# Performance work log

Hardware: AMD Instinct MI355X
Metric: run time of the kernel (lower is better)

## Reference

```python
import jax, jax.numpy as jnp
import numpy as np

N = 200000
E = 400000
H = 256
L = 4
FEAT = 10
NUM_BOND_TYPES = 4
VOCAB = 100


def _layernorm(x, g, b, eps=1e-5):
    mu = jnp.mean(x, axis=-1, keepdims=True)
    var = jnp.var(x, axis=-1, keepdims=True)
    return (x - mu) * jax.lax.rsqrt(var + eps) * g + b


def setup_inputs() -> dict:
    key = jax.random.key(0)
    ks = jax.random.split(key, 20)
    s = 0.05
    return {
        "z": jax.random.randint(ks[0], (N,), 0, VOCAB),
        "feat": jax.random.normal(ks[1], (N, FEAT), jnp.float32),
        "edge_index": jax.random.randint(ks[2], (2, E), 0, N),
        "edge_attr": jax.random.uniform(ks[3], (E, NUM_BOND_TYPES), jnp.float32),
        "batch": jnp.sort(jax.random.randint(ks[4], (N,), 0, 512)),
        "emb": jax.random.normal(ks[5], (VOCAB, H), jnp.float32) * s,
        "Wf": jax.random.normal(ks[6], (FEAT, H), jnp.float32) * s,
        "bf": jnp.zeros((H,), jnp.float32),
        "g0": jnp.ones((H,), jnp.float32),
        "b0": jnp.zeros((H,), jnp.float32),
        "We": jax.random.normal(ks[7], (NUM_BOND_TYPES, H), jnp.float32) * s,
        "be": jnp.zeros((H,), jnp.float32),
        "W1": jax.random.normal(ks[8], (L, H, H), jnp.float32) * s,
        "b1": jnp.zeros((L, H), jnp.float32),
        "W2": jax.random.normal(ks[9], (L, H, H), jnp.float32) * s,
        "b2": jnp.zeros((L, H), jnp.float32),
        "ln_g": jnp.ones((L, H), jnp.float32),
        "ln_b": jnp.zeros((L, H), jnp.float32),
    }


def reference(z, feat, edge_index, edge_attr, batch, emb, Wf, bf, g0, b0,
              We, be, W1, b1, W2, b2, ln_g, ln_b):
    act = jax.nn.silu
    # node embedding: silu(Emb[z] + feat @ Wf + bf) -> LayerNorm
    x = _layernorm(act(emb[z] + feat @ Wf + bf), g0, b0)  # [N, H]
    # edge feature projection: silu(edge_attr @ We + be)
    e = act(edge_attr @ We + be)  # [E, H]
    src, dst = edge_index[0], edge_index[1]
    for l in range(L):
        # GINEConv message: relu(x_j + e_ij), sum-aggregated at destination
        m = jax.nn.relu(x[src] + e)  # [E, H]
        agg = jax.ops.segment_sum(m, dst, num_segments=N)  # [N, H]
        h = agg + x  # eps = 0
        h = act(h @ W1[l] + b1[l]) @ W2[l] + b2[l]
        x = _layernorm(x + h, ln_g[l], ln_b[l])
    return x, batch
```

## Files before the change

kernel.cpp:

```cpp
#include <hip/hip_runtime.h>
#include <hip/hip_bf16.h>

#define NN 200000
#define EE 400000
#define HDIM 256
#define LL 4
#define FEAT 10

typedef unsigned short ushort_t;
typedef unsigned char uchar_t;
typedef __attribute__((ext_vector_type(8))) short bf16x8;
typedef __attribute__((ext_vector_type(8))) unsigned short u16x8;
typedef __attribute__((ext_vector_type(2))) float f32x2;
typedef __attribute__((ext_vector_type(4))) float f32x4;
typedef __attribute__((ext_vector_type(4))) unsigned int u32x4;

__device__ inline ushort_t f2bf(float f) {
    unsigned int u = __builtin_bit_cast(unsigned int, f);
    return (ushort_t)((u + 0x7fffu + ((u >> 16) & 1u)) >> 16);
}
__device__ inline float bf2f(ushort_t s) {
    unsigned int u = ((unsigned int)s) << 16;
    return __builtin_bit_cast(float, u);
}
__device__ inline float silu_f(float v) { return v / (1.0f + __expf(-v)); }

__device__ inline void x8_load(const void* base, size_t idx, float* f) {
    uint2 v = ((const uint2*)base)[idx];
    f32x2 a0 = __builtin_amdgcn_cvt_pk_f32_fp8((int)v.x, false);
    f32x2 a1 = __builtin_amdgcn_cvt_pk_f32_fp8((int)v.x, true);
    f32x2 a2 = __builtin_amdgcn_cvt_pk_f32_fp8((int)v.y, false);
    f32x2 a3 = __builtin_amdgcn_cvt_pk_f32_fp8((int)v.y, true);
    f[0]=a0[0]; f[1]=a0[1]; f[2]=a1[0]; f[3]=a1[1];
    f[4]=a2[0]; f[5]=a2[1]; f[6]=a3[0]; f[7]=a3[1];
}
__device__ inline void x8_store(void* base, size_t idx, const float* f) {
    int t0 = __builtin_amdgcn_cvt_pk_fp8_f32(f[0], f[1], 0, false);
    t0 = __builtin_amdgcn_cvt_pk_fp8_f32(f[2], f[3], t0, true);
    int t1 = __builtin_amdgcn_cvt_pk_fp8_f32(f[4], f[5], 0, false);
    t1 = __builtin_amdgcn_cvt_pk_fp8_f32(f[6], f[7], t1, true);
    uint2 o; o.x = (unsigned int)t0; o.y = (unsigned int)t1;
    ((uint2*)base)[idx] = o;
}

__global__ __launch_bounds__(256) void prep_wf_kernel(
    const float* __restrict__ Wf, ushort_t* __restrict__ Wfc)
{
    int idx = blockIdx.x * 256 + threadIdx.x;
    if (idx >= 8192) return;
    int e = idx & 7;
    int lane = (idx >> 3) & 63;
    int nf = (idx >> 9) & 1;
    int w8 = idx >> 10;
    int n = w8 * 32 + nf * 16 + (lane & 15);
    int k = (lane >> 4) * 8 + e;
    Wfc[idx] = (k < FEAT) ? f2bf(Wf[k * HDIM + n]) : (ushort_t)0;
}

__global__ __launch_bounds__(512, 4) void node_init_kernel(
    const int* __restrict__ z, const float* __restrict__ feat,
    const float* __restrict__ emb, const ushort_t* __restrict__ Wfc,
    const float* __restrict__ bfv, const float* __restrict__ g0,
    const float* __restrict__ b0, void* __restrict__ xb)
{
    __shared__ ushort_t sA[64][256];
    __shared__ float sGB[2][HDIM];
    const int tid = threadIdx.x;
    const int m0 = blockIdx.x * 64;
    const int lane = tid & 63;
    const int w = tid >> 6;
    const int lg = lane >> 4, ll = lane & 15;
    const int cb = w * 32;

    if (tid < HDIM) sGB[0][tid] = g0[tid];
    else sGB[1][tid - HDIM] = b0[tid - HDIM];

    f32x4 bvv[2];
    #pragma unroll
    for (int nf = 0; nf < 2; ++nf)
        bvv[nf] = *(const f32x4*)&bfv[cb + nf * 16 + lg * 4];

    bf16x8 wf[2];
    wf[0] = *(const bf16x8*)(Wfc + w * 1024 + lane * 8);
    wf[1] = *(const bf16x8*)(Wfc + w * 1024 + 512 + lane * 8);

    bf16x8 af[4];
    #pragma unroll
    for (int m = 0; m < 4; ++m) {
        int gr = m0 + m * 16 + ll;
        bf16x8 t = {};
        if (lg == 0) {
            #pragma unroll
            for (int j = 0; j < 8; ++j) t[j] = (short)f2bf(feat[gr * FEAT + j]);
        } else if (lg == 1) {
            t[0] = (short)f2bf(feat[gr * FEAT + 8]);
            t[1] = (short)f2bf(feat[gr * FEAT + 9]);
        }
        af[m] = t;
    }

    f32x4 acc[4][2] = {};
    #pragma unroll
    for (int m = 0; m < 4; ++m)
        #pragma unroll
        for (int nf = 0; nf < 2; ++nf)
            acc[m][nf] = __builtin_amdgcn_mfma_f32_16x16x32_bf16(
                wf[nf], af[m], acc[m][nf], 0, 0, 0);

    #pragma unroll
    for (int m = 0; m < 4; ++m) {
        int r = m * 16 + ll, rx = r & 7;
        int zi = z[m0 + r];
        #pragma unroll
        for (int nf = 0; nf < 2; ++nf) {
            int n0 = cb + nf * 16 + lg * 4;
            f32x4 ev = *(const f32x4*)&emb[(size_t)zi * HDIM + n0];
            int chunk = ((cb + nf * 16) >> 3) + (lg >> 1);
            int celloff = ((chunk ^ rx) << 3) + (lg & 1) * 4;
            ushort4 o;
            o.x = f2bf(silu_f(acc[m][nf][0] + ev[0] + bvv[nf][0]));
            o.y = f2bf(silu_f(acc[m][nf][1] + ev[1] + bvv[nf][1]));
            o.z = f2bf(silu_f(acc[m][nf][2] + ev[2] + bvv[nf][2]));
            o.w = f2bf(silu_f(acc[m][nf][3] + ev[3] + bvv[nf][3]));
            *(ushort4*)&sA[r][celloff] = o;
        }
    }
    __syncthreads();

    {
        int rr = tid >> 3, kk = tid & 7;
        int rot = (kk + rr) & 7;
        u16x8 v8[4];
        float s = 0.f, q = 0.f;
        #pragma unroll
        for (int i = 0; i < 4; ++i) {
            int slot = rot + 8 * i;
            v8[i] = *(const u16x8*)&sA[rr][slot << 3];
            #pragma unroll
            for (int j = 0; j < 8; ++j) {
                float v = bf2f(v8[i][j]);
                s += v; q += v * v;
            }
        }
        #pragma unroll
        for (int o = 1; o < 8; o <<= 1) {
            s += __shfl_xor(s, o, 64);
            q += __shfl_xor(q, o, 64);
        }
        float mu = s * (1.0f / HDIM);
        float var = q * (1.0f / HDIM) - mu * mu;
        float rs = rsqrtf(var + 1e-5f);
        size_t rows = ((size_t)(m0 + rr)) << 5;
        #pragma unroll
        for (int i = 0; i < 4; ++i) {
            int slot = rot + 8 * i;
            int chunk = slot ^ (rr & 7);
            float ov[8];
            #pragma unroll
            for (int j = 0; j < 8; ++j)
                ov[j] = (bf2f(v8[i][j]) - mu) * rs * sGB[0][chunk * 8 + j]
                        + sGB[1][chunk * 8 + j];
            x8_store(xb, rows + slot, ov);
        }
    }
}

__global__ __launch_bounds__(256) void batch_out_kernel(
    const int* __restrict__ batch, float* __restrict__ out)
{
    int i = blockIdx.x * 256 + threadIdx.x;
    if (i < NN) out[i] = (float)batch[i];
}

__global__ __launch_bounds__(256) void hist_kernel(const int* __restrict__ ei, int* __restrict__ deg)
{
    int i = blockIdx.x * 256 + threadIdx.x;
    if (i < EE) atomicAdd(&deg[ei[EE + i]], 1);
}

__global__ __launch_bounds__(256) void scan_blocks_kernel(
    const int* __restrict__ deg, int* __restrict__ off, int* __restrict__ psum)
{
    int blk = blockIdx.x, t = threadIdx.x;
    int base = blk * 1024 + t * 4;
    int v[4];
    #pragma unroll
    for (int i = 0; i < 4; ++i) v[i] = (base + i < NN) ? deg[base + i] : 0;
    int s = v[0] + v[1] + v[2] + v[3];
    int lane = t & 63, w = t >> 6;
    int ps = s;
    #pragma unroll
    for (int o = 1; o < 64; o <<= 1) { int u = __shfl_up(ps, o, 64); if (lane >= o) ps += u; }
    __shared__ int wt[4];
    if (lane == 63) wt[w] = ps;
    __syncthreads();
    int wbase = 0;
    for (int k = 0; k < w; ++k) wbase += wt[k];
    int run = wbase + ps - s;
    #pragma unroll
    for (int i = 0; i < 4; ++i) {
        if (base + i < NN) off[base + i] = run;
        run += v[i];
    }
    if (t == 255) psum[blk] = wbase + ps;
}

__global__ __launch_bounds__(256) void scan_top_kernel(int* __restrict__ psum, int nb)
{
    int t = threadIdx.x;
    int v = (t < nb) ? psum[t] : 0;
    int lane = t & 63, w = t >> 6;
    int ps = v;
    #pragma unroll
    for (int o = 1; o < 64; o <<= 1) { int u = __shfl_up(ps, o, 64); if (lane >= o) ps += u; }
    __shared__ int wt[4];
    if (lane == 63) wt[w] = ps;
    __syncthreads();
    int wbase = 0;
    for (int k = 0; k < w; ++k) wbase += wt[k];
    if (t < nb) psum[t] = wbase + ps - v;
}

__global__ __launch_bounds__(256) void scan_add_kernel(
    int* __restrict__ off, const int* __restrict__ psum, int* __restrict__ cursor)
{
    int i = blockIdx.x * 256 + threadIdx.x;
    if (i < NN) {
        int o = off[i] + psum[i >> 10];
        off[i] = o;
        cursor[i] = o;
        if (i == NN - 1) off[NN] = EE;
    }
}

__global__ __launch_bounds__(256) void scatter_kernel(
    const int* __restrict__ ei, const float* __restrict__ ea,
    int* __restrict__ cursor, int* __restrict__ srcs, float4* __restrict__ eaf)
{
    int i = blockIdx.x * 256 + threadIdx.x;
    if (i < EE) {
        int dst = ei[EE + i];
        int pos = atomicAdd(&cursor[dst], 1);
        srcs[pos] = ei[i];
        eaf[pos] = ((const float4*)ea)[i];
    }
}

__global__ __launch_bounds__(256) void edge_mlp_kernel(
    const float4* __restrict__ eaf, const float* __restrict__ We,
    const float* __restrict__ be, void* __restrict__ eout)
{
    int p = (blockIdx.x * 256 + threadIdx.x) >> 5;
    if (p >= EE) return;
    int nl = threadIdx.x & 31, c0 = nl * 8;
    float4 av = eaf[p];
    float v[8];
    #pragma unroll
    for (int j = 0; j < 8; ++j) {
        float t = be[c0 + j] + av.x * We[c0 + j] + av.y * We[HDIM + c0 + j]
                + av.z * We[2 * HDIM + c0 + j] + av.w * We[3 * HDIM + c0 + j];
        v[j] = silu_f(t);
    }
    x8_store(eout, ((size_t)p << 5) + nl, v);
}

__global__ __launch_bounds__(256) void prep_w_kernel(
    const float* __restrict__ W1, const float* __restrict__ W2,
    uchar_t* __restrict__ Wc1, uchar_t* __restrict__ Wc2)
{
    int idx = blockIdx.x * 256 + threadIdx.x;
    int which = idx >> 18;
    int rem = idx & 0x3FFFF;
    int l = rem >> 16;
    int t = rem & 0xFFFF;
    int e = t & 7;
    int lane = (t >> 3) & 63;
    int nf = (t >> 9) & 1;
    int w8 = (t >> 10) & 7;
    int c = (t >> 13) & 7;
    int n = w8 * 32 + nf * 16 + (lane & 15);
    int k = c * 32 + (lane >> 4) * 8 + e;
    const float* W = which ? W2 : W1;
    float v = W[l * 65536 + k * 256 + n];
    uchar_t* Wc = which ? Wc2 : Wc1;
    int pk = __builtin_amdgcn_cvt_pk_fp8_f32(v, v, 0, false);
    Wc[rem] = (uchar_t)(pk & 0xFF);
}

template<int USE_E>
__global__ __launch_bounds__(256) void agg_kernel(
    const int* __restrict__ off, const int* __restrict__ srcs,
    const void* __restrict__ eprec, const float4* __restrict__ eaf,
    const float* __restrict__ We, const float* __restrict__ be,
    const void* __restrict__ xin, void* __restrict__ U)
{
    const int gstride = (gridDim.x * 256) >> 5;
    const int gid0 = (blockIdx.x * 256 + threadIdx.x) >> 5;
    const int nl = threadIdx.x & 31, c0 = nl * 8;
    float wv[4][8], bev[8];
    if (!USE_E) {
        #pragma unroll
        for (int r4 = 0; r4 < 4; ++r4)
            #pragma unroll
            for (int j = 0; j < 8; ++j) wv[r4][j] = We[r4 * HDIM + c0 + j];
        #pragma unroll
        for (int j = 0; j < 8; ++j) bev[j] = be[c0 + j];
    }

    for (int n = gid0; n < NN; n += gstride) {
        float acc[8];
        x8_load(xin, (((size_t)n) << 5) + (nl ^ (n & 7)), acc);
        int beg = off[n], end = off[n + 1];
        if (USE_E) {
            for (int p = beg; p < end; ++p) {
                int src = srcs[p];
                float xg[8], ev[8];
                x8_load(xin, (((size_t)src) << 5) + (nl ^ (src & 7)), xg);
                x8_load(eprec, ((size_t)p << 5) + nl, ev);
                #pragma unroll
                for (int j = 0; j < 8; ++j)
                    acc[j] += fmaxf(xg[j] + ev[j], 0.f);
            }
        } else {
            for (int p = beg; p < end; ++p) {
                int src = srcs[p];
                float4 av = eaf[p];
                float xg[8];
                x8_load(xin, (((size_t)src) << 5) + (nl ^ (src & 7)), xg);
                #pragma unroll
                for (int j = 0; j < 8; ++j) {
                    float e = silu_f(bev[j] + av.x * wv[0][j] + av.y * wv[1][j]
                                            + av.z * wv[2][j] + av.w * wv[3][j]);
                    acc[j] += fmaxf(xg[j] + e, 0.f);
                }
            }
        }
        x8_store(U, (((size_t)n) << 5) + (nl ^ (n & 7)), acc);
    }
}

template<int LAST>
__global__ __launch_bounds__(512, 4) void mlp_kernel(
    const void* __restrict__ U, const uchar_t* __restrict__ Wc1,
    const uchar_t* __restrict__ Wc2, const float* __restrict__ b1,
    const float* __restrict__ b2, const float* __restrict__ lng,
    const float* __restrict__ lnb, const void* __restrict__ xin,
    void* __restrict__ xout, float* __restrict__ xf32)
{
    __shared__ uchar_t sF[64][256];
    __shared__ float sGB[2][HDIM];
    const int tid = threadIdx.x;
    const int m0 = blockIdx.x * 64;
    const int lane = tid & 63;
    const int w = tid >> 6;
    const int lg = lane >> 4, ll = lane & 15;
    const int cb = w * 32;

    if (tid < HDIM) sGB[0][tid] = lng[tid];
    else sGB[1][tid - HDIM] = lnb[tid - HDIM];

    f32x4 bv1v[2], bv2v[2];
    #pragma unroll
    for (int nf = 0; nf < 2; ++nf) {
        int nb = cb + nf * 16 + lg * 4;
        bv1v[nf] = *(const f32x4*)&b1[nb];
        bv2v[nf] = *(const f32x4*)&b2[nb];
    }

    {
        const uint2* Uq = (const uint2*)U + (((size_t)m0) << 5);
        uint2* sQ = (uint2*)&sF[0][0];
        #pragma unroll
        for (int it = 0; it < 4; ++it) {
            int idx = tid + it * 512;
            sQ[idx] = Uq[idx];
        }
    }
    __syncthreads();

    f32x4 acc[4][2] = {};
    const uchar_t* wp1 = Wc1 + w * 1024 + lane * 8;
    const uchar_t* wp2 = Wc2 + w * 1024 + lane * 8;
    long long wbuf[2][2];
    wbuf[0][0] = *(const long long*)(wp1);
    wbuf[0][1] = *(const long long*)(wp1 + 512);

    #pragma unroll
    for (int p = 0; p < 8; ++p) {
        const uchar_t* nsrc = (p < 7) ? (wp1 + (p + 1) * 8192) : wp2;
        wbuf[(p + 1) & 1][0] = *(const long long*)(nsrc);
        wbuf[(p + 1) & 1][1] = *(const long long*)(nsrc + 512);
        long long af[4];
        #pragma unroll
        for (int m = 0; m < 4; ++m) {
            int r = m * 16 + ll;
            af[m] = *(const long long*)&sF[r][(((p * 4 + lg) ^ (r & 7)) << 3)];
        }
        #pragma unroll
        for (int m = 0; m < 4; ++m)
            #pragma unroll
            for (int nf = 0; nf < 2; ++nf)
                acc[m][nf] = __builtin_amdgcn_mfma_f32_16x16x32_fp8_fp8(
                    wbuf[p & 1][nf], af[m], acc[m][nf], 0, 0, 0);
    }
    __syncthreads();

    #pragma unroll
    for (int m = 0; m < 4; ++m) {
        int r = m * 16 + ll, rx = r & 7;
        #pragma unroll
        for (int nf = 0; nf < 2; ++nf) {
            int chunk = ((cb + nf * 16) >> 3) + (lg >> 1);
            int boff = ((chunk ^ rx) << 3) + (lg & 1) * 4;
            float v0 = silu_f(acc[m][nf][0] + bv1v[nf][0]);
            float v1 = silu_f(acc[m][nf][1] + bv1v[nf][1]);
            float v2 = silu_f(acc[m][nf][2] + bv1v[nf][2]);
            float v3 = silu_f(acc[m][nf][3] + bv1v[nf][3]);
            int pk = __builtin_amdgcn_cvt_pk_fp8_f32(v0, v1, 0, false);
            pk = __builtin_amdgcn_cvt_pk_fp8_f32(v2, v3, pk, true);
            *(unsigned int*)&sF[r][boff] = (unsigned int)pk;
            acc[m][nf][0] = 0.f; acc[m][nf][1] = 0.f;
            acc[m][nf][2] = 0.f; acc[m][nf][3] = 0.f;
        }
    }
    __syncthreads();

    #pragma unroll
    for (int p = 0; p < 8; ++p) {
        if (p < 7) {
            wbuf[(p + 1) & 1][0] = *(const long long*)(wp2 + (p + 1) * 8192);
            wbuf[(p + 1) & 1][1] = *(const long long*)(wp2 + (p + 1) * 8192 + 512);
        }
        long long af[4];
        #pragma unroll
        for (int m = 0; m < 4; ++m) {
            int r = m * 16 + ll;
            af[m] = *(const long long*)&sF[r][(((p * 4 + lg) ^ (r & 7)) << 3)];
        }
        #pragma unroll
        for (int m = 0; m < 4; ++m)
            #pragma unroll
            for (int nf = 0; nf < 2; ++nf)
                acc[m][nf] = __builtin_amdgcn_mfma_f32_16x16x32_fp8_fp8(
                    wbuf[p & 1][nf], af[m], acc[m][nf], 0, 0, 0);
    }
    __syncthreads();

    #pragma unroll
    for (int m = 0; m < 4; ++m) {
        int r = m * 16 + ll, rx = r & 7;
        #pragma unroll
        for (int nf = 0; nf < 2; ++nf) {
            int chunk = ((cb + nf * 16) >> 3) + (lg >> 1);
            int boff = ((chunk ^ rx) << 3) + (lg & 1) * 4;
            float v0 = acc[m][nf][0] + bv2v[nf][0];
            float v1 = acc[m][nf][1] + bv2v[nf][1];
            float v2 = acc[m][nf][2] + bv2v[nf][2];
            float v3 = acc[m][nf][3] + bv2v[nf][3];
            int pk = __builtin_amdgcn_cvt_pk_fp8_f32(v0, v1, 0, false);
            pk = __builtin_amdgcn_cvt_pk_fp8_f32(v2, v3, pk, true);
            *(unsigned int*)&sF[r][boff] = (unsigned int)pk;
        }
    }
    __syncthreads();

    {
        int rr = tid >> 3, kk = tid & 7;
        int rot = (kk + rr) & 7;
        size_t rows = ((size_t)(m0 + rr)) << 5;
        float vv[4][8];
        float s = 0.f, q = 0.f;
        #pragma unroll
        for (int i = 0; i < 4; ++i) {
            int slot = rot + 8 * i;
            uint2 hq = *(const uint2*)&sF[rr][slot << 3];
            f32x2 h0 = __builtin_amdgcn_cvt_pk_f32_fp8((int)hq.x, false);
            f32x2 h1 = __builtin_amdgcn_cvt_pk_f32_fp8((int)hq.x, true);
            f32x2 h2 = __builtin_amdgcn_cvt_pk_f32_fp8((int)hq.y, false);
            f32x2 h3 = __builtin_amdgcn_cvt_pk_f32_fp8((int)hq.y, true);
            float hf[8] = {h0[0], h0[1], h1[0], h1[1], h2[0], h2[1], h3[0], h3[1]};
            float x8[8];
            x8_load(xin, rows + slot, x8);
            #pragma unroll
            for (int j = 0; j < 8; ++j) {
                float v = hf[j] + x8[j];
                vv[i][j] = v;
                s += v; q += v * v;
            }
        }
        #pragma unroll
        for (int o = 1; o < 8; o <<= 1) {
            s += __shfl_xor(s, o, 64);
            q += __shfl_xor(q, o, 64);
        }
        float mu = s * (1.0f / HDIM);
        float var = q * (1.0f / HDIM) - mu * mu;
        float rs = rsqrtf(var + 1e-5f);
        #pragma unroll
        for (int i = 0; i < 4; ++i) {
            int slot = rot + 8 * i;
            int chunk = slot ^ (rr & 7);
            if (LAST) {
                float* xrow = xf32 + (((size_t)(m0 + rr)) << 8);
                f32x4 o0, o1;
                #pragma unroll
                for (int j = 0; j < 4; ++j) {
                    o0[j] = (vv[i][j] - mu) * rs * sGB[0][chunk * 8 + j]
                            + sGB[1][chunk * 8 + j];
                    o1[j] = (vv[i][4 + j] - mu) * rs * sGB[0][chunk * 8 + 4 + j]
                            + sGB[1][chunk * 8 + 4 + j];
                }
                *(f32x4*)&xrow[chunk * 8] = o0;
                *(f32x4*)&xrow[chunk * 8 + 4] = o1;
            } else {
                float ov[8];
                #pragma unroll
                for (int j = 0; j < 8; ++j)
                    ov[j] = (vv[i][j] - mu) * rs * sGB[0][chunk * 8 + j]
                            + sGB[1][chunk * 8 + j];
                x8_store(xout, rows + slot, ov);
            }
        }
    }
}

extern "C" void kernel_launch(void* const* d_in, const int* in_sizes, int n_in,
                              void* d_out, int out_size, void* d_ws, size_t ws_size,
                              hipStream_t stream)
{
    const int*   z    = (const int*)d_in[0];
    const float* feat = (const float*)d_in[1];
    const int*   ei   = (const int*)d_in[2];
    const float* ea   = (const float*)d_in[3];
    const int*   batch= (const int*)d_in[4];
    const float* emb  = (const float*)d_in[5];
    const float* Wf   = (const float*)d_in[6];
    const float* bfv  = (const float*)d_in[7];
    const float* g0   = (const float*)d_in[8];
    const float* b0   = (const float*)d_in[9];
    const float* We   = (const float*)d_in[10];
    const float* be   = (const float*)d_in[11];
    const float* W1   = (const float*)d_in[12];
    const float* b1   = (const float*)d_in[13];
    const float* W2   = (const float*)d_in[14];
    const float* b2   = (const float*)d_in[15];
    const float* lng  = (const float*)d_in[16];
    const float* lnb  = (const float*)d_in[17];

    float* x    = (float*)d_out;
    float* outb = (float*)d_out + (size_t)NN * HDIM;

    const size_t XBYTES = (size_t)NN * 256;
    const size_t EBYTES = (size_t)EE * 256;
    const size_t WBYTES = (size_t)LL * 65536;

    char* ws = (char*)d_ws;
    size_t o = 0;
    void* xb0 = (void*)(ws + o); o += XBYTES;
    void* xb1 = (void*)(ws + o); o += XBYTES;
    void* Ubuf = (void*)(ws + o); o += XBYTES;
    float4* eaf = (float4*)(ws + o); o += (size_t)EE * 16;
    int* srcs = (int*)(ws + o); o += (size_t)EE * 4;
    int* off = (int*)(ws + o); o += (size_t)(NN + 4) * 4;
    int* cursor = (int*)(ws + o); o += (size_t)NN * 4;
    int* deg = (int*)(ws + o); o += (size_t)NN * 4;
    int* psum = (int*)(ws + o); o += 1024;
    uchar_t* Wc1 = (uchar_t*)(ws + o); o += WBYTES;
    uchar_t* Wc2 = (uchar_t*)(ws + o); o += WBYTES;
    ushort_t* Wfc = (ushort_t*)(ws + o); o += 16384;
    void* eprec = (void*)(ws + o); o += EBYTES;
    const int use_e = (ws_size >= o) ? 1 : 0;

    prep_w_kernel<<<2048, 256, 0, stream>>>(W1, W2, Wc1, Wc2);
    prep_wf_kernel<<<32, 256, 0, stream>>>(Wf, Wfc);
    batch_out_kernel<<<782, 256, 0, stream>>>(batch, outb);
    node_init_kernel<<<NN / 64, 512, 0, stream>>>(z, feat, emb, Wfc, bfv, g0, b0, xb0);

    hipMemsetAsync(deg, 0, NN * sizeof(int), stream);
    hist_kernel<<<1563, 256, 0, stream>>>(ei, deg);
    scan_blocks_kernel<<<196, 256, 0, stream>>>(deg, off, psum);
    scan_top_kernel<<<1, 256, 0, stream>>>(psum, 196);
    scan_add_kernel<<<782, 256, 0, stream>>>(off, psum, cursor);
    scatter_kernel<<<1563, 256, 0, stream>>>(ei, ea, cursor, srcs, eaf);
    if (use_e)
        edge_mlp_kernel<<<EE / 8, 256, 0, stream>>>(eaf, We, be, eprec);

    void* xbuf[2] = {xb0, xb1};
    for (int l = 0; l < LL; ++l) {
        void* xin  = xbuf[l & 1];
        void* xout = xbuf[(l + 1) & 1];
        if (use_e)
            agg_kernel<1><<<2048, 256, 0, stream>>>(off, srcs, eprec, eaf, We, be, xin, Ubuf);
        else
            agg_kernel<0><<<2048, 256, 0, stream>>>(off, srcs, eprec, eaf, We, be, xin, Ubuf);
        if (l == LL - 1) {
            mlp_kernel<1><<<NN / 64, 512, 0, stream>>>(
                Ubuf, Wc1 + l * 65536, Wc2 + l * 65536, b1 + l * HDIM, b2 + l * HDIM,
                lng + l * HDIM, lnb + l * HDIM, xin, xout, x);
        } else {
            mlp_kernel<0><<<NN / 64, 512, 0, stream>>>(
                Ubuf, Wc1 + l * 65536, Wc2 + l * 65536, b1 + l * HDIM, b2 + l * HDIM,
                lng + l * HDIM, lnb + l * HDIM, xin, xout, nullptr);
        }
    }
}
```

Before: 712.6 us.

## Fuse edge MLP into scatter, deepen weight prefetch, double agg grid

```diff
diff --git a/kernel.cpp b/kernel.cpp
--- a/kernel.cpp
+++ b/kernel.cpp
@@ -235,25 +235,25 @@
 
 __global__ __launch_bounds__(256) void scatter_kernel(
     const int* __restrict__ ei, const float* __restrict__ ea,
-    int* __restrict__ cursor, int* __restrict__ srcs, float4* __restrict__ eaf)
-{
-    int i = blockIdx.x * 256 + threadIdx.x;
-    if (i < EE) {
-        int dst = ei[EE + i];
-        int pos = atomicAdd(&cursor[dst], 1);
-        srcs[pos] = ei[i];
-        eaf[pos] = ((const float4*)ea)[i];
-    }
-}
-
-__global__ __launch_bounds__(256) void edge_mlp_kernel(
-    const float4* __restrict__ eaf, const float* __restrict__ We,
-    const float* __restrict__ be, void* __restrict__ eout)
-{
-    int p = (blockIdx.x * 256 + threadIdx.x) >> 5;
-    if (p >= EE) return;
+    const float* __restrict__ We, const float* __restrict__ be,
+    int* __restrict__ cursor, int* __restrict__ srcs,
+    float4* __restrict__ eaf, void* __restrict__ e16)
+{
+    int g = (blockIdx.x * 256 + threadIdx.x) >> 5;
+    if (g >= EE) return;
+    int lane = threadIdx.x & 63;
     int nl = threadIdx.x & 31, c0 = nl * 8;
-    float4 av = eaf[p];
+    float4 av = ((const float4*)ea)[g];
+    int pos = 0;
+    if (nl == 0) {
+        int dst = ei[EE + g];
+        pos = atomicAdd(&cursor[dst], 1);
+    }
+    pos = __shfl(pos, lane & 32, 64);
+    if (nl == 0) {
+        srcs[pos] = ei[g];
+        eaf[pos] = av;
+    }
     float v[8];
     #pragma unroll
     for (int j = 0; j < 8; ++j) {
@@ -261,7 +261,7 @@
                 + av.z * We[2 * HDIM + c0 + j] + av.w * We[3 * HDIM + c0 + j];
         v[j] = silu_f(t);
     }
-    x8_store(eout, ((size_t)p << 5) + nl, v);
+    x8_store(e16, ((size_t)pos << 5) + nl, v);
 }
 
 __global__ __launch_bounds__(256) void prep_w_kernel(
@@ -384,12 +384,11 @@
     long long wbuf[2][2];
     wbuf[0][0] = *(const long long*)(wp1);
     wbuf[0][1] = *(const long long*)(wp1 + 512);
+    wbuf[1][0] = *(const long long*)(wp1 + 8192);
+    wbuf[1][1] = *(const long long*)(wp1 + 8192 + 512);
 
     #pragma unroll
     for (int p = 0; p < 8; ++p) {
-        const uchar_t* nsrc = (p < 7) ? (wp1 + (p + 1) * 8192) : wp2;
-        wbuf[(p + 1) & 1][0] = *(const long long*)(nsrc);
-        wbuf[(p + 1) & 1][1] = *(const long long*)(nsrc + 512);
         long long af[4];
         #pragma unroll
         for (int m = 0; m < 4; ++m) {
@@ -402,6 +401,9 @@
             for (int nf = 0; nf < 2; ++nf)
                 acc[m][nf] = __builtin_amdgcn_mfma_f32_16x16x32_fp8_fp8(
                     wbuf[p & 1][nf], af[m], acc[m][nf], 0, 0, 0);
+        const uchar_t* nsrc = (p < 6) ? (wp1 + (p + 2) * 8192) : (wp2 + (p - 6) * 8192);
+        wbuf[p & 1][0] = *(const long long*)(nsrc);
+        wbuf[p & 1][1] = *(const long long*)(nsrc + 512);
     }
     __syncthreads();
 
@@ -427,10 +429,6 @@
 
     #pragma unroll
     for (int p = 0; p < 8; ++p) {
-        if (p < 7) {
-            wbuf[(p + 1) & 1][0] = *(const long long*)(wp2 + (p + 1) * 8192);
-            wbuf[(p + 1) & 1][1] = *(const long long*)(wp2 + (p + 1) * 8192 + 512);
-        }
         long long af[4];
         #pragma unroll
         for (int m = 0; m < 4; ++m) {
@@ -443,6 +441,11 @@
             for (int nf = 0; nf < 2; ++nf)
                 acc[m][nf] = __builtin_amdgcn_mfma_f32_16x16x32_fp8_fp8(
                     wbuf[p & 1][nf], af[m], acc[m][nf], 0, 0, 0);
+        if (p < 6) {
+            const uchar_t* nsrc = wp2 + (p + 2) * 8192;
+            wbuf[p & 1][0] = *(const long long*)(nsrc);
+            wbuf[p & 1][1] = *(const long long*)(nsrc + 512);
+        }
     }
     __syncthreads();
 
@@ -581,18 +584,16 @@
     scan_blocks_kernel<<<196, 256, 0, stream>>>(deg, off, psum);
     scan_top_kernel<<<1, 256, 0, stream>>>(psum, 196);
     scan_add_kernel<<<782, 256, 0, stream>>>(off, psum, cursor);
-    scatter_kernel<<<1563, 256, 0, stream>>>(ei, ea, cursor, srcs, eaf);
-    if (use_e)
-        edge_mlp_kernel<<<EE / 8, 256, 0, stream>>>(eaf, We, be, eprec);
+    scatter_kernel<<<EE * 32 / 256, 256, 0, stream>>>(ei, ea, We, be, cursor, srcs, eaf, eprec);
 
     void* xbuf[2] = {xb0, xb1};
     for (int l = 0; l < LL; ++l) {
         void* xin  = xbuf[l & 1];
         void* xout = xbuf[(l + 1) & 1];
         if (use_e)
-            agg_kernel<1><<<2048, 256, 0, stream>>>(off, srcs, eprec, eaf, We, be, xin, Ubuf);
+            agg_kernel<1><<<4096, 256, 0, stream>>>(off, srcs, eprec, eaf, We, be, xin, Ubuf);
         else
-            agg_kernel<0><<<2048, 256, 0, stream>>>(off, srcs, eprec, eaf, We, be, xin, Ubuf);
+            agg_kernel<0><<<4096, 256, 0, stream>>>(off, srcs, eprec, eaf, We, be, xin, Ubuf);
         if (l == LL - 1) {
             mlp_kernel<1><<<NN / 64, 512, 0, stream>>>(
                 Ubuf, Wc1 + l * 65536, Wc2 + l * 65536, b1 + l * HDIM, b2 + l * HDIM,
```

Result: slower. 735.4 us (+3.2%).
